# Kernel tuning notes

Hardware: AMD Instinct MI355X
Metric: run time of the kernel (lower is better)

## Reference

```python
import jax, jax.numpy as jnp
import numpy as np

N, D, H, DH, FF, NE, NNZ = 4096, 128, 2, 64, 256, 2048, 65536
EPS = 1e-5

def layer_norm(x, g, b):
    m = jnp.mean(x, axis=-1, keepdims=True)
    v = jnp.var(x, axis=-1, keepdims=True)
    return (x - m) / jnp.sqrt(v + EPS) * g + b

def setup_inputs() -> dict:
    key = jax.random.key(0)
    ks = jax.random.split(key, 24)
    s = 0.05
    node_idx = jax.random.randint(ks[1], (NNZ,), 0, N)
    he_idx = jax.random.randint(ks[2], (NNZ,), 0, NE)
    return {
        "x": jax.random.normal(ks[0], (N, D), dtype=jnp.float32),
        "edge": jnp.stack([node_idx, he_idx]).astype(jnp.int64),
        "Wq": jax.random.normal(ks[3], (D, D)) * s, "bq": jnp.zeros((D,)),
        "Wk": jax.random.normal(ks[4], (D, D)) * s, "bk": jnp.zeros((D,)),
        "Wv": jax.random.normal(ks[5], (D, D)) * s, "bv": jnp.zeros((D,)),
        "Wo": jax.random.normal(ks[6], (D, D)) * s, "bo": jnp.zeros((D,)),
        "g_ln1": jnp.ones((D,)), "b_ln1": jnp.zeros((D,)),
        "W1": jax.random.normal(ks[7], (D, FF)) * s, "bf1": jnp.zeros((FF,)),
        "W2": jax.random.normal(ks[8], (FF, D)) * s, "bf2": jnp.zeros((D,)),
        "g_ln2": jnp.ones((D,)), "b_ln2": jnp.zeros((D,)),
        "Wh": jax.random.normal(ks[9], (D, D)) * s, "bh": jnp.zeros((D,)),
    }

def reference(x, edge, Wq, bq, Wk, bk, Wv, bv, Wo, bo, g_ln1, b_ln1,
              W1, bf1, W2, bf2, g_ln2, b_ln2, Wh, bh):
    # dropout layers run in eval mode (identity) for a deterministic reference
    def mha_block(h):
        q = (h @ Wq + bq).reshape(N, H, DH)
        k = (h @ Wk + bk).reshape(N, H, DH)
        v = (h @ Wv + bv).reshape(N, H, DH)
        scores = jnp.einsum('nhd,mhd->hnm', q, k) / jnp.sqrt(jnp.float32(DH))
        attn = jax.nn.softmax(scores, axis=-1)            # [H,N,N]
        o = jnp.einsum('hnm,mhd->nhd', attn, v).reshape(N, D)
        return layer_norm(h + o @ Wo + bo, g_ln1, b_ln1)

    def ff_block(h):
        z = jax.nn.sigmoid(h @ W1 + bf1)
        return layer_norm(h + z @ W2 + bf2, g_ln2, b_ln2)

    h = ff_block(mha_block(x))
    h = ff_block(mha_block(h))

    # HypergraphConv: out = D^{-1} H B^{-1} H^T (X Theta) + bias
    node_idx = edge[0]
    he_idx = edge[1]
    xt = h @ Wh                                            # [N,D]
    ones = jnp.ones((NNZ,), dtype=xt.dtype)
    Bdeg = jax.ops.segment_sum(ones, he_idx, num_segments=NE)
    Binv = jnp.where(Bdeg > 0, 1.0 / Bdeg, 0.0)
    Ddeg = jax.ops.segment_sum(ones, node_idx, num_segments=N)
    Dinv = jnp.where(Ddeg > 0, 1.0 / Ddeg, 0.0)
    e = jax.ops.segment_sum(xt[node_idx], he_idx, num_segments=NE) * Binv[:, None]
    out = jax.ops.segment_sum(e[he_idx], node_idx, num_segments=N) * Dinv[:, None] + bh
    return jax.nn.relu(out)
```

## Files before the change

kernel.cpp:

```cpp
#include <hip/hip_runtime.h>
#include <hip/hip_bf16.h>
#include <cstddef>

#define N_NODES 4096
#define DIM     128
#define NHEAD   2
#define DHEAD   64
#define FFDIM   256
#define NEDGE   2048
#define NNZ_E   65536
#define NSPLIT  8

typedef __attribute__((ext_vector_type(8))) short bf16x8;
typedef __attribute__((ext_vector_type(4))) float f32x4;
typedef unsigned short u16;

__device__ __forceinline__ u16 f2b(float f) {
    unsigned u = __float_as_uint(f);
    return (u16)((u + 0x7FFFu + ((u >> 16) & 1u)) >> 16);
}
__device__ __forceinline__ float b2f_bits(u16 h) {
    return __uint_as_float(((unsigned)h) << 16);
}
__device__ __forceinline__ unsigned cvtpk(float a, float b) {
    unsigned r;
    asm("v_cvt_pk_bf16_f32 %0, %1, %2" : "=v"(r) : "v"(a), "v"(b));
    return r;
}

__global__ void prep(const float* __restrict__ x, float* __restrict__ h,
                     u16* __restrict__ hh, u16* __restrict__ hl,
                     const float* W0, const float* W1, const float* W2,
                     const float* W3, const float* W4, const float* W5,
                     const float* W6,
                     u16* P0, u16* P1, u16* P2, u16* P3, u16* P4, u16* P5, u16* P6,
                     const int* __restrict__ edge_raw,
                     int* __restrict__ nidx, int* __restrict__ hidx,
                     int* __restrict__ cnt_e, int* __restrict__ cnt_n) {
    const int bx = blockIdx.x;
    if (bx < 512) {
        int i4 = bx * 256 + threadIdx.x;
        float4 f4 = ((const float4*)x)[i4];
        ((float4*)h)[i4] = f4;
        ushort4 hi4, lo4;
        hi4.x = f2b(f4.x); lo4.x = f2b(f4.x - b2f_bits(hi4.x));
        hi4.y = f2b(f4.y); lo4.y = f2b(f4.y - b2f_bits(hi4.y));
        hi4.z = f2b(f4.z); lo4.z = f2b(f4.z - b2f_bits(hi4.z));
        hi4.w = f2b(f4.w); lo4.w = f2b(f4.w - b2f_bits(hi4.w));
        ((ushort4*)hh)[i4] = hi4;
        ((ushort4*)hl)[i4] = lo4;
        return;
    }
    if (bx >= 584) {
        __shared__ int is64_s;
        if (threadIdx.x < 64) {
            int v = edge_raw[2 * threadIdx.x + 1];
            unsigned long long bal = __ballot(v != 0);
            if (threadIdx.x == 0) is64_s = (bal == 0ull) ? 1 : 0;
        }
        __syncthreads();
        const int is64 = is64_s;
        int i = (bx - 584) * 256 + threadIdx.x;
        if (i < NNZ_E) {
            int ni = (is64 ? edge_raw[2 * i]             : edge_raw[i])         & (N_NODES - 1);
            int he = (is64 ? edge_raw[2 * NNZ_E + 2 * i] : edge_raw[NNZ_E + i]) & (NEDGE - 1);
            nidx[i] = ni;
            hidx[i] = he;
            atomicAdd(&cnt_n[ni], 1);
            atomicAdd(&cnt_e[he], 1);
        }
        return;
    }
    const int p = bx - 512;
    int mid, blk0;
    if (p < 40)      { mid = p >> 3; blk0 = p & 7;  }
    else if (p < 56) { mid = 5;      blk0 = p - 40; }
    else             { mid = 6;      blk0 = p - 56; }
    const float* W; u16* P; int nsh, knc;
    switch (mid) {
        case 0: W = W0; P = P0; nsh = 7; knc = 16384; break;
        case 1: W = W1; P = P1; nsh = 7; knc = 16384; break;
        case 2: W = W2; P = P2; nsh = 7; knc = 16384; break;
        case 3: W = W3; P = P3; nsh = 7; knc = 16384; break;
        case 4: W = W4; P = P4; nsh = 7; knc = 16384; break;
        case 5: W = W5; P = P5; nsh = 8; knc = 32768; break;
        default: W = W6; P = P6; nsh = 7; knc = 32768; break;
    }
    const int NC = 1 << nsh;
    int idx = blk0 * 256 + threadIdx.x;
    int k8 = idx >> nsh, n = idx & (NC - 1);
    size_t wb = ((size_t)k8 * 8) * NC + n;
    float f0 = W[wb];          float f1 = W[wb + NC];
    float f2 = W[wb + 2 * NC]; float f3 = W[wb + 3 * NC];
    float f4 = W[wb + 4 * NC]; float f5 = W[wb + 5 * NC];
    float f6 = W[wb + 6 * NC]; float f7 = W[wb + 7 * NC];
    uint4 hi;
    hi.x = cvtpk(f0, f1); hi.y = cvtpk(f2, f3);
    hi.z = cvtpk(f4, f5); hi.w = cvtpk(f6, f7);
    uint4 lo;
    lo.x = cvtpk(f0 - __uint_as_float(hi.x << 16), f1 - __uint_as_float(hi.x & 0xFFFF0000u));
    lo.y = cvtpk(f2 - __uint_as_float(hi.y << 16), f3 - __uint_as_float(hi.y & 0xFFFF0000u));
    lo.z = cvtpk(f4 - __uint_as_float(hi.z << 16), f5 - __uint_as_float(hi.z & 0xFFFF0000u));
    lo.w = cvtpk(f6 - __uint_as_float(hi.w << 16), f7 - __uint_as_float(hi.w & 0xFFFF0000u));
    size_t o = ((size_t)k8 * NC + n) * 8;
    *(uint4*)&P[o]       = hi;
    *(uint4*)&P[knc + o] = lo;
}

__global__ __launch_bounds__(256) void qkv_mfma(const u16* __restrict__ Ah,
                                                const u16* __restrict__ Al,
                                                const u16* __restrict__ Wq,
                                                const u16* __restrict__ Wk,
                                                const u16* __restrict__ Wv,
                                                const float* __restrict__ bq,
                                                const float* __restrict__ bk,
                                                const float* __restrict__ bv,
                                                u16* __restrict__ qb,
                                                u16* __restrict__ kb,
                                                u16* __restrict__ vtb) {
    const int K = 128, NC = 128;
    const int tid = threadIdx.x, w = tid >> 6, lane = tid & 63;
    const int qi = lane & 15, gi = lane >> 4;
    const int row0 = blockIdx.x * 64 + w * 16;
    const int sel = blockIdx.y >> 2;
    const int col0 = (blockIdx.y & 3) * 32;
    const u16* Wp = (sel == 0) ? Wq : (sel == 1) ? Wk : Wv;
    const float* bias = (sel == 0) ? bq : (sel == 1) ? bk : bv;
    const u16* Wlo = Wp + (size_t)K * NC;

    f32x4 aca[2], acb[2];
#pragma unroll
    for (int c = 0; c < 2; ++c) {
        aca[c] = (f32x4){0.f, 0.f, 0.f, 0.f};
        acb[c] = (f32x4){0.f, 0.f, 0.f, 0.f};
    }

#pragma unroll
    for (int kc = 0; kc < K / 32; ++kc) {
        const int k0 = kc * 32;
        const size_t ao = (size_t)(row0 + qi) * K + k0 + gi * 8;
        bf16x8 ah = *(const bf16x8*)(Ah + ao);
        bf16x8 al = *(const bf16x8*)(Al + ao);
#pragma unroll
        for (int c = 0; c < 2; ++c) {
            f32x4& acc = (kc < 2) ? aca[c] : acb[c];
            const size_t wo = ((size_t)(k0 / 8 + gi) * NC + col0 + c * 16 + qi) * 8;
            bf16x8 wh = *(const bf16x8*)(Wp + wo);
            bf16x8 wl = *(const bf16x8*)(Wlo + wo);
            acc = __builtin_amdgcn_mfma_f32_16x16x32_bf16(ah, wh, acc, 0, 0, 0);
            acc = __builtin_amdgcn_mfma_f32_16x16x32_bf16(al, wh, acc, 0, 0, 0);
            acc = __builtin_amdgcn_mfma_f32_16x16x32_bf16(ah, wl, acc, 0, 0, 0);
        }
    }

#pragma unroll
    for (int c = 0; c < 2; ++c) {
        f32x4 acc = aca[c] + acb[c];
        const int col = col0 + c * 16 + qi;
        const int hh = col >> 6, d = col & 63;
        float bv_ = bias[col];
        if (sel < 2) {
            u16* dst = (sel == 0) ? qb : kb;
#pragma unroll
            for (int r = 0; r < 4; ++r) {
                const int grow = row0 + gi * 4 + r;
                dst[((size_t)hh * N_NODES + grow) * 64 + d] = f2b(acc[r] + bv_);
            }
        } else {
            const int grow0 = row0 + gi * 4;
            uint2 pw;
            pw.x = cvtpk(acc[0] + bv_, acc[1] + bv_);
            pw.y = cvtpk(acc[2] + bv_, acc[3] + bv_);
            *(uint2*)&vtb[((size_t)hh * 64 + d) * N_NODES + grow0] = pw;
        }
    }
}

#define ROWP 72
__global__ __launch_bounds__(512, 4) void attn_mfma(const u16* __restrict__ qb,
                                                    const u16* __restrict__ kb,
                                                    const u16* __restrict__ vtb,
                                                    float* __restrict__ op,
                                                    float* __restrict__ mll,
                                                    const int* __restrict__ cnt_e,
                                                    const int* __restrict__ cnt_n,
                                                    int* __restrict__ off_e,
                                                    int* __restrict__ off_n,
                                                    int* __restrict__ cur_e,
                                                    int* __restrict__ cur_n) {
    __shared__ __align__(16) u16 k_s[2][64 * ROWP];
    __shared__ __align__(16) u16 vt_s[2][64 * ROWP];
    __shared__ __align__(16) u16 p_s[8][16 * ROWP];

    if (blockIdx.x >= 32) {
        if (blockIdx.y == 0 && blockIdx.z < 2) {
            int* sbuf = (int*)&k_s[0][0];
            const int he_side = (blockIdx.z == 0);
            const int n = he_side ? NEDGE : N_NODES;
            const int* cnt = he_side ? cnt_e : cnt_n;
            int* off = he_side ? off_e : off_n;
            int* cur = he_side ? cur_e : cur_n;
            for (int i = threadIdx.x; i < n; i += 512) sbuf[i] = cnt[i];
            __syncthreads();
            for (int st = 1; st < n; st <<= 1) {
                int v[8]; int nj = 0;
                for (int i = threadIdx.x; i < n; i += 512) v[nj++] = (i >= st) ? sbuf[i - st] : 0;
                __syncthreads();
                nj = 0;
                for (int i = threadIdx.x; i < n; i += 512) sbuf[i] += v[nj++];
                __syncthreads();
            }
            for (int i = threadIdx.x; i < n; i += 512) { off[i + 1] = sbuf[i]; cur[i] = 0; }
            if (threadIdx.x == 0) off[0] = 0;
        }
        return;
    }

    const int h = blockIdx.y;
    const int s = blockIdx.z;
    const int row0 = blockIdx.x * 128;
    const int tid = threadIdx.x;
    const int w = tid >> 6, lane = tid & 63;
    const int qi = lane & 15, gi = lane >> 4;
    const float CE = 0.18033688011f;

    const u16* qrow = qb + ((size_t)h * N_NODES + row0 + w * 16 + qi) * 64 + gi * 8;
    bf16x8 qf0 = *(const bf16x8*)qrow;
    bf16x8 qf1 = *(const bf16x8*)(qrow + 32);

    f32x4 oc[4];
#pragma unroll
    for (int i = 0; i < 4; ++i) oc[i] = (f32x4){0.f, 0.f, 0.f, 0.f};
    float l_run = 0.f;

    const u16* kbh = kb + (size_t)h * N_NODES * 64;
    const u16* vth = vtb + (size_t)h * 64 * N_NODES;

    const int nt0 = s * (N_NODES / 64 / NSPLIT);
    const int nt1 = nt0 + N_NODES / 64 / NSPLIT;
    const int r = tid >> 3, ss = tid & 7;

    {
        const u16* ksrc = kbh + nt0 * 64 * 64;
        *(uint4*)&k_s[0][r * ROWP + ss * 8]  = *(const uint4*)(ksrc + tid * 8);
        *(uint4*)&vt_s[0][r * ROWP + ss * 8] = *(const uint4*)(vth + (size_t)r * N_NODES + nt0 * 64 + ss * 8);
    }
    __syncthreads();
    int cur = 0;

    for (int kt = nt0; kt < nt1; ++kt) {
        uint4 knx, vnx;
        const bool more = (kt + 1 < nt1);
        if (more) {
            const u16* ksrc = kbh + (kt + 1) * 64 * 64;
            knx = *(const uint4*)(ksrc + tid * 8);
            vnx = *(const uint4*)(vth + (size_t)r * N_NODES + (kt + 1) * 64 + ss * 8);
        }

        f32x4 sc[4];
        __builtin_amdgcn_s_setprio(1);
#pragma unroll
        for (int t = 0; t < 4; ++t) {
            const u16* krow = &k_s[cur][(t * 16 + qi) * ROWP + gi * 8];
            bf16x8 ka0 = *(const bf16x8*)krow;
            bf16x8 ka1 = *(const bf16x8*)(krow + 32);
            f32x4 z = (f32x4){0.f, 0.f, 0.f, 0.f};
            z = __builtin_amdgcn_mfma_f32_16x16x32_bf16(ka0, qf0, z, 0, 0, 0);
            sc[t] = __builtin_amdgcn_mfma_f32_16x16x32_bf16(ka1, qf1, z, 0, 0, 0);
        }
        __builtin_amdgcn_s_setprio(0);

        float psum = 0.f;
#pragma unroll
        for (int t = 0; t < 4; ++t) {
            float p0 = exp2f(sc[t][0] * CE);
            float p1 = exp2f(sc[t][1] * CE);
            float p2 = exp2f(sc[t][2] * CE);
            float p3 = exp2f(sc[t][3] * CE);
            psum += (p0 + p1) + (p2 + p3);
            uint2 pw;
            pw.x = cvtpk(p0, p1);
            pw.y = cvtpk(p2, p3);
            *(uint2*)&p_s[w][qi * ROWP + t * 16 + gi * 4] = pw;
        }
        psum += __shfl_xor(psum, 16);
        psum += __shfl_xor(psum, 32);
        l_run += psum;

        const u16* prow = &p_s[w][qi * ROWP];
        bf16x8 pa0 = *(const bf16x8*)(prow + gi * 8);
        bf16x8 pa1 = *(const bf16x8*)(prow + 32 + gi * 8);
        __builtin_amdgcn_s_setprio(1);
#pragma unroll
        for (int d = 0; d < 4; ++d) {
            const u16* vrow = &vt_s[cur][(d * 16 + qi) * ROWP + gi * 8];
            bf16x8 vb0 = *(const bf16x8*)vrow;
            bf16x8 vb1 = *(const bf16x8*)(vrow + 32);
            oc[d] = __builtin_amdgcn_mfma_f32_16x16x32_bf16(pa0, vb0, oc[d], 0, 0, 0);
            oc[d] = __builtin_amdgcn_mfma_f32_16x16x32_bf16(pa1, vb1, oc[d], 0, 0, 0);
        }
        __builtin_amdgcn_s_setprio(0);

        if (more) {
            *(uint4*)&k_s[cur ^ 1][r * ROWP + ss * 8]  = knx;
            *(uint4*)&vt_s[cur ^ 1][r * ROWP + ss * 8] = vnx;
        }
        __syncthreads();
        cur ^= 1;
    }

    float* opd = op + (size_t)s * N_NODES * 128;
#pragma unroll
    for (int d = 0; d < 4; ++d) {
        size_t cb = h * 64 + d * 16 + qi;
        opd[(size_t)(row0 + w * 16 + gi * 4 + 0) * 128 + cb] = oc[d][0];
        opd[(size_t)(row0 + w * 16 + gi * 4 + 1) * 128 + cb] = oc[d][1];
        opd[(size_t)(row0 + w * 16 + gi * 4 + 2) * 128 + cb] = oc[d][2];
        opd[(size_t)(row0 + w * 16 + gi * 4 + 3) * 128 + cb] = oc[d][3];
    }
    if (gi == 0) {
        size_t mi = (size_t)s * NHEAD * N_NODES + (size_t)h * N_NODES + row0 + w * 16 + qi;
        mll[mi] = l_run;
    }
}

#define ROWA 136
#define ROWZ 264
#define ROWH 132
template<int DO_QKV>
__global__ __launch_bounds__(512) void mega_layer(
        const float* __restrict__ op, const float* __restrict__ mll,
        const u16* __restrict__ wp_o, const float* __restrict__ bo,
        float* __restrict__ h,
        const float* __restrict__ g1, const float* __restrict__ b1,
        const u16* __restrict__ wp_1, const float* __restrict__ bf1,
        const u16* __restrict__ wp_2, const float* __restrict__ bf2,
        const float* __restrict__ g2, const float* __restrict__ b2,
        const u16* __restrict__ wp_q, const u16* __restrict__ wp_k,
        const u16* __restrict__ wp_v,
        const float* __restrict__ bq, const float* __restrict__ bk,
        const float* __restrict__ bv,
        u16* __restrict__ qb, u16* __restrict__ kb, u16* __restrict__ vtb,
        const u16* __restrict__ wp_h, float* __restrict__ xt,
        const int* __restrict__ nidx, const int* __restrict__ hidx,
        const int* __restrict__ off_e, const int* __restrict__ off_n,
        int* __restrict__ cur_e, int* __restrict__ cur_n,
        int* __restrict__ csr_e, int* __restrict__ csr_n) {
    if (DO_QKV && blockIdx.x >= N_NODES / 16) {
        int i = (blockIdx.x - N_NODES / 16) * 512 + threadIdx.x;
        if (i < NNZ_E) {
            int ni = nidx[i], he = hidx[i];
            int p = atomicAdd(&cur_e[he], 1);
            csr_e[off_e[he] + p] = ni;
            int q = atomicAdd(&cur_n[ni], 1);
            csr_n[off_n[ni] + q] = he;
        }
        return;
    }
    __shared__ __align__(16) u16 zbuf[16 * ROWZ * 2];
    __shared__ __align__(16) u16 hp_hi[16 * ROWA];
    __shared__ __align__(16) u16 hp_lo[16 * ROWA];
    __shared__ float hln[16 * ROWH];
    __shared__ float Linv_s[32];
    __shared__ float wsum[8][16], wsq[8][16];
    const int tid = threadIdx.x, w = tid >> 6, lane = tid & 63;
    const int qi = lane & 15, gi = lane >> 4;
    const int row0 = blockIdx.x * 16;
    u16* a_hi = zbuf;
    u16* a_lo = zbuf + 16 * ROWA;
    u16* z_hi = zbuf;
    u16* z_lo = zbuf + 16 * ROWZ;

    if (tid < 32) {
        int r = tid >> 1, hd = tid & 1;
        size_t mb = (size_t)hd * N_NODES + row0 + r;
        float L = 0.f;
#pragma unroll
        for (int s = 0; s < NSPLIT; ++s)
            L += mll[mb + (size_t)s * NHEAD * N_NODES];
        Linv_s[tid] = 1.f / L;
    }
    __syncthreads();

    {
        int r = tid >> 5, c4 = tid & 31;
        int hd = c4 >> 4;
        float4 O = {0.f, 0.f, 0.f, 0.f};
        const float4* opr = (const float4*)(op + (size_t)(row0 + r) * 128) + c4;
#pragma unroll
        for (int s = 0; s < NSPLIT; ++s) {
            float4 v = opr[(size_t)s * N_NODES * 32];
            O.x += v.x; O.y += v.y; O.z += v.z; O.w += v.w;
        }
        float li = Linv_s[r * 2 + hd];
        O.x *= li; O.y *= li; O.z *= li; O.w *= li;
        uint2 hi, lo;
        hi.x = cvtpk(O.x, O.y); hi.y = cvtpk(O.z, O.w);
        lo.x = cvtpk(O.x - __uint_as_float(hi.x << 16),
                     O.y - __uint_as_float(hi.x & 0xFFFF0000u));
        lo.y = cvtpk(O.z - __uint_as_float(hi.y << 16),
                     O.w - __uint_as_float(hi.y & 0xFFFF0000u));
        *(uint2*)&a_hi[r * ROWA + c4 * 4] = hi;
        *(uint2*)&a_lo[r * ROWA + c4 * 4] = lo;
    }
    __syncthreads();

    {
        const u16* Wlo = wp_o + (size_t)128 * 128;
        f32x4 ac0 = (f32x4){0.f, 0.f, 0.f, 0.f};
        f32x4 ac1 = (f32x4){0.f, 0.f, 0.f, 0.f};
        const int col0 = w * 16;
#pragma unroll
        for (int kc = 0; kc < 4; ++kc) {
            const int k0 = kc * 32;
            f32x4& acc = (kc < 2) ? ac0 : ac1;
            bf16x8 ah = *(const bf16x8*)&a_hi[qi * ROWA + k0 + gi * 8];
            bf16x8 al = *(const bf16x8*)&a_lo[qi * ROWA + k0 + gi * 8];
            const size_t wo = ((size_t)(k0 / 8 + gi) * 128 + col0 + qi) * 8;
            bf16x8 wh = *(const bf16x8*)(wp_o + wo);
            bf16x8 wl = *(const bf16x8*)(Wlo + wo);
            acc = __builtin_amdgcn_mfma_f32_16x16x32_bf16(ah, wh, acc, 0, 0, 0);
            acc = __builtin_amdgcn_mfma_f32_16x16x32_bf16(al, wh, acc, 0, 0, 0);
            acc = __builtin_amdgcn_mfma_f32_16x16x32_bf16(ah, wl, acc, 0, 0, 0);
        }
        f32x4 acc = ac0 + ac1;
        float y[4], rs[4], rq[4];
        const int col = col0 + qi;
        float bvv = bo[col];
#pragma unroll
        for (int r = 0; r < 4; ++r) {
            float v = acc[r] + bvv + h[(size_t)(row0 + gi * 4 + r) * 128 + col];
            y[r] = v;
            rs[r] = v; rq[r] = v * v;
        }
#pragma unroll
        for (int r = 0; r < 4; ++r)
            for (int msk = 1; msk < 16; msk <<= 1) {
                rs[r] += __shfl_xor(rs[r], msk);
                rq[r] += __shfl_xor(rq[r], msk);
            }
        if (qi == 0) {
#pragma unroll
            for (int r = 0; r < 4; ++r) { wsum[w][gi * 4 + r] = rs[r]; wsq[w][gi * 4 + r] = rq[r]; }
        }
        __syncthreads();
#pragma unroll
        for (int r = 0; r < 4; ++r) {
            const int lr = gi * 4 + r;
            float ts = 0.f, tq = 0.f;
#pragma unroll
            for (int ww = 0; ww < 8; ++ww) { ts += wsum[ww][lr]; tq += wsq[ww][lr]; }
            float mean = ts * (1.f / 128.f);
            float var  = tq * (1.f / 128.f) - mean * mean;
            float rstd = rsqrtf(var + 1e-5f);
            float yn = (y[r] - mean) * rstd * g1[col] + b1[col];
            hln[lr * ROWH + col] = yn;
            u16 hi = f2b(yn);
            hp_hi[lr * ROWA + col] = hi;
            hp_lo[lr * ROWA + col] = f2b(yn - b2f_bits(hi));
        }
    }
    __syncthreads();

    {
        const u16* W1lo = wp_1 + (size_t)128 * 256;
        f32x4 acc1[2][2];
#pragma unroll
        for (int t = 0; t < 2; ++t) {
            acc1[t][0] = (f32x4){0.f, 0.f, 0.f, 0.f};
            acc1[t][1] = (f32x4){0.f, 0.f, 0.f, 0.f};
        }
#pragma unroll
        for (int kc = 0; kc < 4; ++kc) {
            const int k0 = kc * 32;
            bf16x8 ah = *(const bf16x8*)&hp_hi[qi * ROWA + k0 + gi * 8];
            bf16x8 al = *(const bf16x8*)&hp_lo[qi * ROWA + k0 + gi * 8];
#pragma unroll
            for (int t = 0; t < 2; ++t) {
                f32x4& acc = acc1[t][kc < 2 ? 0 : 1];
                const size_t wo = ((size_t)(k0 / 8 + gi) * 256 + w * 32 + t * 16 + qi) * 8;
                bf16x8 wh = *(const bf16x8*)(wp_1 + wo);
                bf16x8 wl = *(const bf16x8*)(W1lo + wo);
                acc = __builtin_amdgcn_mfma_f32_16x16x32_bf16(ah, wh, acc, 0, 0, 0);
                acc = __builtin_amdgcn_mfma_f32_16x16x32_bf16(al, wh, acc, 0, 0, 0);
                acc = __builtin_amdgcn_mfma_f32_16x16x32_bf16(ah, wl, acc, 0, 0, 0);
            }
        }
        __syncthreads();
#pragma unroll
        for (int t = 0; t < 2; ++t) {
            f32x4 acc = acc1[t][0] + acc1[t][1];
            const int col = w * 32 + t * 16 + qi;
            float bvv = bf1[col];
#pragma unroll
            for (int r = 0; r < 4; ++r) {
                float v = acc[r] + bvv;
                v = 1.f / (1.f + __expf(-v));
                u16 hi = f2b(v);
                const int zr = gi * 4 + r;
                z_hi[zr * ROWZ + col] = hi;
                z_lo[zr * ROWZ + col] = f2b(v - b2f_bits(hi));
            }
        }
    }
    __syncthreads();

    {
        const u16* W2lo = wp_2 + (size_t)256 * 128;
        f32x4 ac0 = (f32x4){0.f, 0.f, 0.f, 0.f};
        f32x4 ac1 = (f32x4){0.f, 0.f, 0.f, 0.f};
        const int col0 = w * 16;
#pragma unroll
        for (int kc = 0; kc < 8; ++kc) {
            const int k0 = kc * 32;
            f32x4& acc = (kc < 4) ? ac0 : ac1;
            bf16x8 ah = *(const bf16x8*)&z_hi[qi * ROWZ + k0 + gi * 8];
            bf16x8 al = *(const bf16x8*)&z_lo[qi * ROWZ + k0 + gi * 8];
            const size_t wo = ((size_t)(k0 / 8 + gi) * 128 + col0 + qi) * 8;
            bf16x8 wh = *(const bf16x8*)(wp_2 + wo);
            bf16x8 wl = *(const bf16x8*)(W2lo + wo);
            acc = __builtin_amdgcn_mfma_f32_16x16x32_bf16(ah, wh, acc, 0, 0, 0);
            acc = __builtin_amdgcn_mfma_f32_16x16x32_bf16(al, wh, acc, 0, 0, 0);
            acc = __builtin_amdgcn_mfma_f32_16x16x32_bf16(ah, wl, acc, 0, 0, 0);
        }
        f32x4 acc = ac0 + ac1;
        float y[4], rs[4], rq[4];
        const int col = col0 + qi;
        float bvv = bf2[col];
#pragma unroll
        for (int r = 0; r < 4; ++r) {
            float v = acc[r] + bvv + hln[(gi * 4 + r) * ROWH + col];
            y[r] = v;
            rs[r] = v; rq[r] = v * v;
        }
#pragma unroll
        for (int r = 0; r < 4; ++r)
            for (int msk = 1; msk < 16; msk <<= 1) {
                rs[r] += __shfl_xor(rs[r], msk);
                rq[r] += __shfl_xor(rq[r], msk);
            }
        if (qi == 0) {
#pragma unroll
            for (int r = 0; r < 4; ++r) { wsum[w][gi * 4 + r] = rs[r]; wsq[w][gi * 4 + r] = rq[r]; }
        }
        __syncthreads();
#pragma unroll
        for (int r = 0; r < 4; ++r) {
            const int lr = gi * 4 + r;
            float ts = 0.f, tq = 0.f;
#pragma unroll
            for (int ww = 0; ww < 8; ++ww) { ts += wsum[ww][lr]; tq += wsq[ww][lr]; }
            float mean = ts * (1.f / 128.f);
            float var  = tq * (1.f / 128.f) - mean * mean;
            float rstd = rsqrtf(var + 1e-5f);
            float yn = (y[r] - mean) * rstd * g2[col] + b2[col];
            if (DO_QKV) h[(size_t)(row0 + lr) * 128 + col] = yn;
            u16 hi = f2b(yn);
            hp_hi[lr * ROWA + col] = hi;
            hp_lo[lr * ROWA + col] = f2b(yn - b2f_bits(hi));
        }
    }

    if (DO_QKV) {
        __syncthreads();
        const int col0 = w * 16;
#pragma unroll
        for (int sel = 0; sel < 3; ++sel) {
            const u16* Wp = (sel == 0) ? wp_q : (sel == 1) ? wp_k : wp_v;
            const float* bias = (sel == 0) ? bq : (sel == 1) ? bk : bv;
            const u16* Wlo = Wp + (size_t)128 * 128;
            f32x4 ac0 = (f32x4){0.f, 0.f, 0.f, 0.f};
            f32x4 ac1 = (f32x4){0.f, 0.f, 0.f, 0.f};
#pragma unroll
            for (int kc = 0; kc < 4; ++kc) {
                const int k0 = kc * 32;
                f32x4& acc = (kc < 2) ? ac0 : ac1;
                bf16x8 ah = *(const bf16x8*)&hp_hi[qi * ROWA + k0 + gi * 8];
                bf16x8 al = *(const bf16x8*)&hp_lo[qi * ROWA + k0 + gi * 8];
                const size_t wo = ((size_t)(k0 / 8 + gi) * 128 + col0 + qi) * 8;
                bf16x8 wh = *(const bf16x8*)(Wp + wo);
                bf16x8 wl = *(const bf16x8*)(Wlo + wo);
                acc = __builtin_amdgcn_mfma_f32_16x16x32_bf16(ah, wh, acc, 0, 0, 0);
                acc = __builtin_amdgcn_mfma_f32_16x16x32_bf16(al, wh, acc, 0, 0, 0);
                acc = __builtin_amdgcn_mfma_f32_16x16x32_bf16(ah, wl, acc, 0, 0, 0);
            }
            f32x4 acc = ac0 + ac1;
            const int col = col0 + qi;
            const int hh = col >> 6, d = col & 63;
            float bv_ = bias[col];
            if (sel < 2) {
                u16* dst = (sel == 0) ? qb : kb;
#pragma unroll
                for (int r = 0; r < 4; ++r) {
                    const int grow = row0 + gi * 4 + r;
                    dst[((size_t)hh * N_NODES + grow) * 64 + d] = f2b(acc[r] + bv_);
                }
            } else {
                const int grow0 = row0 + gi * 4;
                uint2 pw;
                pw.x = cvtpk(acc[0] + bv_, acc[1] + bv_);
                pw.y = cvtpk(acc[2] + bv_, acc[3] + bv_);
                *(uint2*)&vtb[((size_t)hh * 64 + d) * N_NODES + grow0] = pw;
            }
        }
    } else {
        __syncthreads();
        const u16* Wlo = wp_h + (size_t)128 * 128;
        f32x4 ac0 = (f32x4){0.f, 0.f, 0.f, 0.f};
        f32x4 ac1 = (f32x4){0.f, 0.f, 0.f, 0.f};
        const int col0 = w * 16;
#pragma unroll
        for (int kc = 0; kc < 4; ++kc) {
            const int k0 = kc * 32;
            f32x4& acc = (kc < 2) ? ac0 : ac1;
            bf16x8 ah = *(const bf16x8*)&hp_hi[qi * ROWA + k0 + gi * 8];
            bf16x8 al = *(const bf16x8*)&hp_lo[qi * ROWA + k0 + gi * 8];
            const size_t wo = ((size_t)(k0 / 8 + gi) * 128 + col0 + qi) * 8;
            bf16x8 wh = *(const bf16x8*)(wp_h + wo);
            bf16x8 wl = *(const bf16x8*)(Wlo + wo);
            acc = __builtin_amdgcn_mfma_f32_16x16x32_bf16(ah, wh, acc, 0, 0, 0);
            acc = __builtin_amdgcn_mfma_f32_16x16x32_bf16(al, wh, acc, 0, 0, 0);
            acc = __builtin_amdgcn_mfma_f32_16x16x32_bf16(ah, wl, acc, 0, 0, 0);
        }
        f32x4 acc = ac0 + ac1;
        const int col = col0 + qi;
#pragma unroll
        for (int r = 0; r < 4; ++r)
            xt[(size_t)(row0 + gi * 4 + r) * 128 + col] = acc[r];
    }
}

__global__ __launch_bounds__(128) void gather_e(const int* __restrict__ off_e,
                                                const int* __restrict__ csr_e,
                                                const float* __restrict__ xt,
                                                float* __restrict__ e_sc) {
    __shared__ int ms[128];
    const int he = blockIdx.x, d = threadIdx.x;
    const int beg = off_e[he], end = off_e[he + 1];
    float a0 = 0.f, a1 = 0.f, a2 = 0.f, a3 = 0.f;
    for (int c = beg; c < end; c += 128) {
        int nl = min(128, end - c);
        if (d < nl) ms[d] = csr_e[c + d];
        __syncthreads();
        int j = 0;
        for (; j + 3 < nl; j += 4) {
            a0 += xt[(size_t)ms[j]     * 128 + d];
            a1 += xt[(size_t)ms[j + 1] * 128 + d];
            a2 += xt[(size_t)ms[j + 2] * 128 + d];
            a3 += xt[(size_t)ms[j + 3] * 128 + d];
        }
        for (; j < nl; ++j) a0 += xt[(size_t)ms[j] * 128 + d];
        __syncthreads();
    }
    float binv = (end > beg) ? 1.f / (float)(end - beg) : 0.f;
    e_sc[(size_t)he * 128 + d] = ((a0 + a1) + (a2 + a3)) * binv;
}

__global__ __launch_bounds__(128) void gather_n(const int* __restrict__ off_n,
                                                const int* __restrict__ csr_n,
                                                const float* __restrict__ e_sc,
                                                const float* __restrict__ bh,
                                                float* __restrict__ out) {
    __shared__ int ms[128];
    const int nn = blockIdx.x, d = threadIdx.x;
    const int beg = off_n[nn], end = off_n[nn + 1];
    float a0 = 0.f, a1 = 0.f, a2 = 0.f, a3 = 0.f;
    for (int c = beg; c < end; c += 128) {
        int nl = min(128, end - c);
        if (d < nl) ms[d] = csr_n[c + d];
        __syncthreads();
        int j = 0;
        for (; j + 3 < nl; j += 4) {
            a0 += e_sc[(size_t)ms[j]     * 128 + d];
            a1 += e_sc[(size_t)ms[j + 1] * 128 + d];
            a2 += e_sc[(size_t)ms[j + 2] * 128 + d];
            a3 += e_sc[(size_t)ms[j + 3] * 128 + d];
        }
        for (; j < nl; ++j) a0 += e_sc[(size_t)ms[j] * 128 + d];
        __syncthreads();
    }
    float dinv = (end > beg) ? 1.f / (float)(end - beg) : 0.f;
    float v = ((a0 + a1) + (a2 + a3)) * dinv + bh[d];
    out[(size_t)nn * 128 + d] = v > 0.f ? v : 0.f;
}

extern "C" void kernel_launch(void* const* d_in, const int* in_sizes, int n_in,
                              void* d_out, int out_size, void* d_ws, size_t ws_size,
                              hipStream_t stream) {
    (void)in_sizes; (void)n_in; (void)out_size; (void)ws_size;
    const float* x    = (const float*)d_in[0];
    const int*   edge = (const int*)  d_in[1];
    const float* Wq = (const float*)d_in[2];  const float* bq  = (const float*)d_in[3];
    const float* Wk = (const float*)d_in[4];  const float* bk  = (const float*)d_in[5];
    const float* Wv = (const float*)d_in[6];  const float* bv  = (const float*)d_in[7];
    const float* Wo = (const float*)d_in[8];  const float* bo  = (const float*)d_in[9];
    const float* g1 = (const float*)d_in[10]; const float* b1  = (const float*)d_in[11];
    const float* W1 = (const float*)d_in[12]; const float* bf1 = (const float*)d_in[13];
    const float* W2 = (const float*)d_in[14]; const float* bf2 = (const float*)d_in[15];
    const float* g2 = (const float*)d_in[16]; const float* b2  = (const float*)d_in[17];
    const float* Wh = (const float*)d_in[18]; const float* bh  = (const float*)d_in[19];
    float* out = (float*)d_out;

    float* B = (float*)d_ws;
    float* h    = B;
    u16*   h_hi = (u16*)(B + 524288);
    u16*   h_lo = (u16*)(B + 786432);
    u16*   qb   = (u16*)(B + 1048576);
    u16*   kb   = (u16*)(B + 1310720);
    u16*   vtb  = (u16*)(B + 1835008);
    float* op   = B + 2097152;
    float* mll  = B + 6291456;
    float* xt   = B + 6946816;
    float* e_sc = B + 7471104;
    u16*   wp_q = (u16*)(B + 8519680);
    u16*   wp_k = (u16*)(B + 8536064);
    u16*   wp_v = (u16*)(B + 8552448);
    u16*   wp_o = (u16*)(B + 8568832);
    u16*   wp_h = (u16*)(B + 8585216);
    u16*   wp_1 = (u16*)(B + 8601600);
    u16*   wp_2 = (u16*)(B + 8634368);
    int*   cur_e = (int*)(B + 9328640);
    int*   cur_n = (int*)(B + 9330688);
    int*   off_e = (int*)(B + 9334784);
    int*   off_n = (int*)(B + 9336840);
    int*   csr_e = (int*)(B + 9340944);
    int*   csr_n = (int*)(B + 9406480);
    int*   cnt_e = (int*)(B + 9472016);
    int*   cnt_n = (int*)(B + 9474064);
    int*   nidx  = (int*)(B + 9478160);
    int*   hidx  = (int*)(B + 9543696);

    hipMemsetAsync(cnt_e, 0, (NEDGE + N_NODES) * sizeof(int), stream);

    prep<<<840, 256, 0, stream>>>(x, h, h_hi, h_lo,
                                  Wq, Wk, Wv, Wo, Wh, W1, W2,
                                  wp_q, wp_k, wp_v, wp_o, wp_h, wp_1, wp_2,
                                  edge, nidx, hidx, cnt_e, cnt_n);

    qkv_mfma<<<dim3(64, 12), 256, 0, stream>>>(h_hi, h_lo, wp_q, wp_k, wp_v,
                                               bq, bk, bv, qb, kb, vtb);
    attn_mfma<<<dim3(33, NHEAD, NSPLIT), 512, 0, stream>>>(qb, kb, vtb, op, mll,
                                                           cnt_e, cnt_n, off_e, off_n,
                                                           cur_e, cur_n);
    mega_layer<1><<<N_NODES / 16 + 128, 512, 0, stream>>>(op, mll, wp_o, bo, h, g1, b1,
                                                    wp_1, bf1, wp_2, bf2, g2, b2,
                                                    wp_q, wp_k, wp_v, bq, bk, bv,
                                                    qb, kb, vtb, wp_h, xt,
                                                    nidx, hidx, off_e, off_n,
                                                    cur_e, cur_n, csr_e, csr_n);
    attn_mfma<<<dim3(32, NHEAD, NSPLIT), 512, 0, stream>>>(qb, kb, vtb, op, mll,
                                                           cnt_e, cnt_n, off_e, off_n,
                                                           cur_e, cur_n);
    mega_layer<0><<<N_NODES / 16, 512, 0, stream>>>(op, mll, wp_o, bo, h, g1, b1,
                                                    wp_1, bf1, wp_2, bf2, g2, b2,
                                                    nullptr, nullptr, nullptr,
                                                    nullptr, nullptr, nullptr,
                                                    nullptr, nullptr, nullptr,
                                                    wp_h, xt,
                                                    nullptr, nullptr, nullptr, nullptr,
                                                    nullptr, nullptr, nullptr, nullptr);

    gather_e<<<NEDGE, 128, 0, stream>>>(off_e, csr_e, xt, e_sc);
    gather_n<<<N_NODES, 128, 0, stream>>>(off_n, csr_n, e_sc, bh, out);
}
```

Baseline: 214.5 us.

## Load attention K/V fragments directly from global memory instead of LDS staging

The attention kernel no longer stages K and V^T tiles through double-buffered shared memory. Each wave now reads its MFMA operand fragments straight from global memory, and the per-tile __syncthreads is gone. This cuts LDS use and block-wide barriers, and the prefix-scan scratch moves into the remaining p_s buffer. The cost is that all 8 waves in a block fetch the same K/V data through L1/L2, and there is no explicit prefetch left to hide global load latency.

```diff
diff --git a/kernel.cpp b/kernel.cpp
--- a/kernel.cpp
+++ b/kernel.cpp
@@ -188,13 +188,11 @@
                                                     int* __restrict__ off_n,
                                                     int* __restrict__ cur_e,
                                                     int* __restrict__ cur_n) {
-    __shared__ __align__(16) u16 k_s[2][64 * ROWP];
-    __shared__ __align__(16) u16 vt_s[2][64 * ROWP];
     __shared__ __align__(16) u16 p_s[8][16 * ROWP];
 
     if (blockIdx.x >= 32) {
         if (blockIdx.y == 0 && blockIdx.z < 2) {
-            int* sbuf = (int*)&k_s[0][0];
+            int* sbuf = (int*)&p_s[0][0];
             const int he_side = (blockIdx.z == 0);
             const int n = he_side ? NEDGE : N_NODES;
             const int* cnt = he_side ? cnt_e : cnt_n;
@@ -233,35 +231,19 @@
     for (int i = 0; i < 4; ++i) oc[i] = (f32x4){0.f, 0.f, 0.f, 0.f};
     float l_run = 0.f;
 
-    const u16* kbh = kb + (size_t)h * N_NODES * 64;
-    const u16* vth = vtb + (size_t)h * 64 * N_NODES;
+    const u16* kfb = kb + (size_t)h * N_NODES * 64 + (size_t)qi * 64 + gi * 8;
+    const u16* vfb = vtb + (size_t)h * 64 * N_NODES + (size_t)qi * N_NODES + gi * 8;
 
     const int nt0 = s * (N_NODES / 64 / NSPLIT);
     const int nt1 = nt0 + N_NODES / 64 / NSPLIT;
-    const int r = tid >> 3, ss = tid & 7;
-
-    {
-        const u16* ksrc = kbh + nt0 * 64 * 64;
-        *(uint4*)&k_s[0][r * ROWP + ss * 8]  = *(const uint4*)(ksrc + tid * 8);
-        *(uint4*)&vt_s[0][r * ROWP + ss * 8] = *(const uint4*)(vth + (size_t)r * N_NODES + nt0 * 64 + ss * 8);
-    }
-    __syncthreads();
-    int cur = 0;
 
     for (int kt = nt0; kt < nt1; ++kt) {
-        uint4 knx, vnx;
-        const bool more = (kt + 1 < nt1);
-        if (more) {
-            const u16* ksrc = kbh + (kt + 1) * 64 * 64;
-            knx = *(const uint4*)(ksrc + tid * 8);
-            vnx = *(const uint4*)(vth + (size_t)r * N_NODES + (kt + 1) * 64 + ss * 8);
-        }
-
         f32x4 sc[4];
+        const u16* kt_base = kfb + (size_t)kt * 64 * 64;
         __builtin_amdgcn_s_setprio(1);
 #pragma unroll
         for (int t = 0; t < 4; ++t) {
-            const u16* krow = &k_s[cur][(t * 16 + qi) * ROWP + gi * 8];
+            const u16* krow = kt_base + (size_t)t * 16 * 64;
             bf16x8 ka0 = *(const bf16x8*)krow;
             bf16x8 ka1 = *(const bf16x8*)(krow + 32);
             f32x4 z = (f32x4){0.f, 0.f, 0.f, 0.f};
@@ -290,23 +272,17 @@
         const u16* prow = &p_s[w][qi * ROWP];
         bf16x8 pa0 = *(const bf16x8*)(prow + gi * 8);
         bf16x8 pa1 = *(const bf16x8*)(prow + 32 + gi * 8);
+        const u16* vt_base = vfb + (size_t)kt * 64;
         __builtin_amdgcn_s_setprio(1);
 #pragma unroll
         for (int d = 0; d < 4; ++d) {
-            const u16* vrow = &vt_s[cur][(d * 16 + qi) * ROWP + gi * 8];
+            const u16* vrow = vt_base + (size_t)d * 16 * N_NODES;
             bf16x8 vb0 = *(const bf16x8*)vrow;
             bf16x8 vb1 = *(const bf16x8*)(vrow + 32);
             oc[d] = __builtin_amdgcn_mfma_f32_16x16x32_bf16(pa0, vb0, oc[d], 0, 0, 0);
             oc[d] = __builtin_amdgcn_mfma_f32_16x16x32_bf16(pa1, vb1, oc[d], 0, 0, 0);
         }
         __builtin_amdgcn_s_setprio(0);
-
-        if (more) {
-            *(uint4*)&k_s[cur ^ 1][r * ROWP + ss * 8]  = knx;
-            *(uint4*)&vt_s[cur ^ 1][r * ROWP + ss * 8] = vnx;
-        }
-        __syncthreads();
-        cur ^= 1;
     }
 
     float* opd = op + (size_t)s * N_NODES * 128;
```

New measurement: 311.7 us. 1.45x slower.
